# Optimization experiments

Measured on AMD Instinct MI355X. Metric: run time of the kernel, lower is better.

The kernel has to match this reference:

```python
import jax, jax.numpy as jnp
import numpy as np
from jax import lax

B, FCH, H, W = 2, 48, 512, 512
WNUM, PATCH = 1, 8
DEG = 180.0 / np.pi
# well-conditioned, slightly asymmetric fallback Mueller matrix for masked (non-physical) pixels
_SAFE = np.array([[1.0, 0.02, 0.01, 0.005],
                  [0.0, 0.95, 0.05, 0.0],
                  [0.0, -0.05, 0.90, 0.04],
                  [0.0, 0.0, -0.04, 0.85]], dtype=np.float32)


def setup_inputs():
    key = jax.random.key(0)
    x = 0.5 * jax.random.normal(key, (B, FCH, H, W), dtype=jnp.float32)
    eye = jnp.eye(4, dtype=jnp.float32).reshape(16)
    # bias intensity frames and both calibration matrices toward 2*I so per-pixel
    # 4x4 systems are well conditioned and M is near-physical
    boost = jnp.concatenate([2.0 * eye, 2.0 * eye, 2.0 * eye])[None, :, None, None]
    return {"x": x + boost}


def _charpoly_mask(M):
    # Cloude realizability test: characteristic-polynomial coefficients of the
    # Hermitian coherency matrix must all be >= 0 (all eigenvalues >= 0).
    s = jnp.stack([jnp.eye(2, dtype=jnp.complex64),
                   jnp.array([[1, 0], [0, -1]], jnp.complex64),
                   jnp.array([[0, 1], [1, 0]], jnp.complex64),
                   jnp.array([[0, -1j], [1j, 0]], jnp.complex64)])
    Bk = jnp.einsum('iab,jcd->ijacbd', s, s).reshape(16, 4, 4)  # kron(sigma_i, sigma_j)
    Hc = 0.25 * jnp.einsum('...k,kab->...ab', M.reshape(M.shape[:-2] + (16,)).astype(jnp.complex64), Bk)
    tr1 = jnp.trace(Hc, axis1=-2, axis2=-1).real
    H2 = Hc @ Hc
    tr2 = jnp.trace(H2, axis1=-2, axis2=-1).real
    tr3 = jnp.trace(H2 @ Hc, axis1=-2, axis2=-1).real
    c2 = 0.5 * (tr1 ** 2 - tr2)
    c3 = (tr1 ** 3 - 3.0 * tr1 * tr2 + 2.0 * tr3) / 6.0
    c4 = jnp.linalg.det(Hc).real
    return (tr1 >= 0) & (c2 >= 0) & (c3 >= 0) & (c4 >= 0)


def _compute_mm(A, F, Wm, norm=True):
    M = jnp.linalg.solve(A, F)  # A^-1 F
    M = jnp.swapaxes(jnp.linalg.solve(jnp.swapaxes(Wm, -1, -2), jnp.swapaxes(M, -1, -2)), -1, -2)  # ... W^-1
    return M / M[..., 0:1, 0:1] if norm else M


def _lu_chipman(M, mask):
    # Lu-Chipman polar decomposition M = M_delta @ M_R @ M_D (per pixel)
    M = jnp.where(mask[..., None, None], M, jnp.asarray(_SAFE))
    I3 = jnp.eye(3, dtype=M.dtype)
    D = M[..., 0, 1:]  # diattenuation vector
    d2 = jnp.clip(jnp.sum(D * D, -1), 0.0, 1.0 - 1e-6)
    d = jnp.sqrt(d2 + 1e-12)
    sq = jnp.sqrt(1.0 - d2)
    Dh = D / jnp.maximum(d, 1e-6)[..., None]
    mD = sq[..., None, None] * I3 + (1.0 - sq)[..., None, None] * (Dh[..., :, None] * Dh[..., None, :])
    ones = jnp.ones(M.shape[:-2] + (1,), M.dtype)
    MD = jnp.concatenate([jnp.concatenate([ones, D], -1)[..., None, :],
                          jnp.concatenate([D[..., None], mD], -1)], -2)
    Mp = jnp.swapaxes(jnp.linalg.solve(MD, jnp.swapaxes(M, -1, -2)), -1, -2)  # M @ MD^-1 (MD symmetric)
    mp = Mp[..., 1:, 1:]
    mm = mp @ jnp.swapaxes(mp, -1, -2)
    lam = jnp.clip(jnp.linalg.eigvalsh(mm), 1e-12, None)  # ascending
    s1, s2, s3 = jnp.sqrt(lam[..., 2]), jnp.sqrt(lam[..., 1]), jnp.sqrt(lam[..., 0])
    sgn = jnp.where(jnp.linalg.det(mp) < 0, -1.0, 1.0).astype(M.dtype)
    A3 = mm + (s1 * s2 + s2 * s3 + s3 * s1)[..., None, None] * I3 + 1e-6 * I3
    B3 = (s1 + s2 + s3)[..., None, None] * mm + (s1 * s2 * s3)[..., None, None] * I3
    mdel = sgn[..., None, None] * jnp.linalg.solve(A3, B3)
    Pdel = (M[..., 1:, 0] - jnp.einsum('...ij,...j->...i', M[..., 1:, 1:], D)) / (1.0 - d2)[..., None]
    top = jnp.concatenate([ones, jnp.zeros(M.shape[:-2] + (3,), M.dtype)], -1)[..., None, :]
    Mdel = jnp.concatenate([top, jnp.concatenate([Pdel[..., None], mdel], -1)], -2)
    MR = jnp.linalg.solve(Mdel + 1e-6 * jnp.eye(4, dtype=M.dtype), Mp)
    return MD, MR, Mdel


def _polarimetry(MD, MR, Mdel):
    clipc = lambda t: jnp.clip(t, -1.0 + 1e-6, 1.0 - 1e-6)
    D = MD[..., 0, 1:]
    totD = jnp.sqrt(jnp.sum(D * D, -1) + 1e-12)
    linD = jnp.sqrt(D[..., 0] ** 2 + D[..., 1] ** 2 + 1e-12)
    cirD = jnp.abs(D[..., 2])
    totR = jnp.arccos(clipc(jnp.trace(MR, axis1=-2, axis2=-1) / 2.0 - 1.0)) * DEG
    mR = MR[..., 1:, 1:]
    linR = jnp.arccos(clipc(jnp.sqrt((mR[..., 0, 0] + mR[..., 1, 1]) ** 2
                                     + (mR[..., 1, 0] - mR[..., 0, 1]) ** 2 + 1e-12) - 1.0)) * DEG
    cirR = 0.5 * jnp.arctan2(mR[..., 1, 0] - mR[..., 0, 1], mR[..., 0, 0] + mR[..., 1, 1]) * DEG
    # azimuth of linear retardance from retardance-vector components (r1, r2)
    azi = jnp.mod(0.5 * jnp.arctan2(mR[..., 2, 0] - mR[..., 0, 2], mR[..., 1, 2] - mR[..., 2, 1]) * DEG, 180.0)
    dazi = jnp.mod(0.5 * jnp.arctan2(D[..., 1], D[..., 0]) * DEG, 180.0)
    totP = 1.0 - jnp.abs(jnp.trace(Mdel[..., 1:, 1:], axis1=-2, axis2=-1)) / 3.0
    # p[:,0]=diattenuation, p[:,6]=linear retardance, p[:,7]=azimuth, p[:,-1]=depolarization
    return jnp.stack([totD, linD, cirD, totR, cirR, dazi, linR, azi, totP], axis=1)


def _rolling_circstd(a_deg, patch):
    # circstd(a/180*pi, high=pi, low=0) over patch x patch sliding windows, back to degrees.
    # circstd reduces to window means of cos/sin of doubled angles -> avg pooling.
    th = a_deg * (2.0 * np.pi / 180.0)
    wsum = lambda t: lax.reduce_window(t, 0.0, lax.add, (1, 1, patch, patch), (1, 1, 1, 1), 'SAME')
    cnt = wsum(jnp.ones_like(a_deg))
    R = jnp.sqrt(wsum(jnp.cos(th)) ** 2 + wsum(jnp.sin(th)) ** 2 + 1e-12) / cnt
    R = jnp.clip(R, 1e-7, 1.0 - 1e-7)
    return 0.5 * jnp.sqrt(-2.0 * jnp.log(R)) * DEG


def _forward(x):
    b, f, h, w = x.shape
    xw = jnp.moveaxis(x.reshape(b, WNUM, f // WNUM, h, w), 2, -1)  # (b, wnum, h, w, 48)
    Fi = xw[..., :16].reshape(b, WNUM, h, w, 4, 4)
    Am = xw[..., 16:32].reshape(b, WNUM, h, w, 4, 4)
    Wm = xw[..., 32:48].reshape(b, WNUM, h, w, 4, 4)
    M = _compute_mm(Am, Fi, Wm, norm=True)
    inten = xw[..., 0]
    imin = inten.min(axis=(1, 2, 3), keepdims=True)
    imax = inten.max(axis=(1, 2, 3), keepdims=True)
    inorm = (inten - imin) / (imax - imin)
    mchan = jnp.moveaxis(M.reshape(b, WNUM, h, w, 16), -1, 2).reshape(b, WNUM * 16, h, w)
    v = lax.stop_gradient(_charpoly_mask(M))
    MD, MR, Mdel = _lu_chipman(M, v)
    p = _polarimetry(MD, MR, Mdel)  # (b, 9, wnum, h, w)
    std = _rolling_circstd(p[:, 7], PATCH)
    # concat order matches forward: intensity, mueller, linr, totp, datt, azimuth, std
    return jnp.concatenate([inorm, mchan, p[:, 6], p[:, 8], p[:, 0], p[:, 7], std], axis=1)


def reference(x):
    return _forward(x)
```

## Files before the change

### kernel.cpp

```cpp
#include <hip/hip_runtime.h>
#include <math.h>

#define B_ 2
#define H_ 512
#define W_ 512
#define HW_ (H_ * W_)
#define NCH_IN 48
#define NCH_OUT 22
#define DEG_ 57.29577951308232f

__device__ __forceinline__ float frcp(float x)  { return __builtin_amdgcn_rcpf(x); }
__device__ __forceinline__ float fsqrtf_(float x){ return __builtin_amdgcn_sqrtf(x); }

__device__ __forceinline__ float fast_acos(float x) {
    float ax = fabsf(x);
    float t = fsqrtf_(fmaxf(1.0f - ax, 0.0f));
    float p = t * (1.5707288f + ax * (-0.2121144f + ax * (0.0742610f + ax * (-0.0187293f))));
    return (x >= 0.0f) ? p : (3.14159265358979f - p);
}

__device__ __forceinline__ float fast_atan2(float y, float x) {
    float ay = fabsf(y), ax = fabsf(x);
    float mx = fmaxf(ax, ay), mn = fminf(ax, ay);
    float a = mn * frcp(fmaxf(mx, 1e-37f));
    float s = a * a;
    float r = a * (0.99997726f + s * (-0.33262347f + s * (0.19354346f +
              s * (-0.11643287f + s * (0.05265332f + s * (-0.01172120f))))));
    if (ay > ax) r = 1.57079632679f - r;
    if (x < 0.0f) r = 3.14159265359f - r;
    return (y < 0.0f) ? -r : r;
}

__device__ __forceinline__ unsigned int fkey(float f) {
    unsigned int u = __float_as_uint(f);
    return (u & 0x80000000u) ? ~u : (u | 0x80000000u);
}
__device__ __forceinline__ float funkey(unsigned int k) {
    return (k & 0x80000000u) ? __uint_as_float(k ^ 0x80000000u) : __uint_as_float(~k);
}

__global__ void init_mm_kernel(unsigned int* mm) {
    mm[0] = 0xFFFFFFFFu; mm[1] = 0u;
    mm[2] = 0xFFFFFFFFu; mm[3] = 0u;
}

__global__ __launch_bounds__(256) void minmax_kernel(const float* __restrict__ x,
                                                     unsigned int* __restrict__ mm) {
    int b = blockIdx.x >> 6;
    int blk = blockIdx.x & 63;
    const float* src = x + (size_t)b * NCH_IN * HW_;
    float lo = INFINITY, hi = -INFINITY;
    for (int i = blk * 256 + threadIdx.x; i < HW_; i += 64 * 256) {
        float v = src[i];
        lo = fminf(lo, v);
        hi = fmaxf(hi, v);
    }
    __shared__ float slo[256], shi[256];
    slo[threadIdx.x] = lo; shi[threadIdx.x] = hi;
    __syncthreads();
    for (int s = 128; s > 0; s >>= 1) {
        if (threadIdx.x < s) {
            slo[threadIdx.x] = fminf(slo[threadIdx.x], slo[threadIdx.x + s]);
            shi[threadIdx.x] = fmaxf(shi[threadIdx.x], shi[threadIdx.x + s]);
        }
        __syncthreads();
    }
    if (threadIdx.x == 0) {
        atomicMin(&mm[2 * b], fkey(slo[0]));
        atomicMax(&mm[2 * b + 1], fkey(shi[0]));
    }
}

__device__ __forceinline__ void solve4(const float A[4][4], const float Bm[4][4], float X[4][4]) {
    float m[4][8];
#pragma unroll
    for (int i = 0; i < 4; i++) {
#pragma unroll
        for (int j = 0; j < 4; j++) { m[i][j] = A[i][j]; m[i][j + 4] = Bm[i][j]; }
    }
#pragma unroll
    for (int k = 0; k < 4; k++) {
#pragma unroll
        for (int r = k + 1; r < 4; r++) {
            bool sw = fabsf(m[r][k]) > fabsf(m[k][k]);
#pragma unroll
            for (int c = 0; c < 8; c++) {
                float a = m[k][c], b = m[r][c];
                m[k][c] = sw ? b : a;
                m[r][c] = sw ? a : b;
            }
        }
        float piv = frcp(m[k][k]);
#pragma unroll
        for (int c = 0; c < 8; c++) m[k][c] *= piv;
#pragma unroll
        for (int r = 0; r < 4; r++) {
            if (r == k) continue;
            float f = m[r][k];
#pragma unroll
            for (int c = 0; c < 8; c++) m[r][c] -= f * m[k][c];
        }
    }
#pragma unroll
    for (int i = 0; i < 4; i++)
#pragma unroll
        for (int j = 0; j < 4; j++) X[i][j] = m[i][j + 4];
}

__device__ __forceinline__ void mul4(const float A[4][4], const float B[4][4], float C[4][4]) {
#pragma unroll
    for (int i = 0; i < 4; i++)
#pragma unroll
        for (int j = 0; j < 4; j++) {
            float s = 0.0f;
#pragma unroll
            for (int k = 0; k < 4; k++) s += A[i][k] * B[k][j];
            C[i][j] = s;
        }
}

__device__ __forceinline__ void inv3(const float A[3][3], float out[3][3]) {
    float c00 = A[1][1] * A[2][2] - A[1][2] * A[2][1];
    float c01 = A[1][2] * A[2][0] - A[1][0] * A[2][2];
    float c02 = A[1][0] * A[2][1] - A[1][1] * A[2][0];
    float det = A[0][0] * c00 + A[0][1] * c01 + A[0][2] * c02;
    float id = frcp(det);
    out[0][0] = c00 * id;
    out[0][1] = (A[0][2] * A[2][1] - A[0][1] * A[2][2]) * id;
    out[0][2] = (A[0][1] * A[1][2] - A[0][2] * A[1][1]) * id;
    out[1][0] = c01 * id;
    out[1][1] = (A[0][0] * A[2][2] - A[0][2] * A[2][0]) * id;
    out[1][2] = (A[0][2] * A[1][0] - A[0][0] * A[1][2]) * id;
    out[2][0] = c02 * id;
    out[2][1] = (A[0][1] * A[2][0] - A[0][0] * A[2][1]) * id;
    out[2][2] = (A[0][0] * A[1][1] - A[0][1] * A[1][0]) * id;
}

__device__ __forceinline__ float det3(const float A[3][3]) {
    return A[0][0] * (A[1][1] * A[2][2] - A[1][2] * A[2][1])
         - A[0][1] * (A[1][0] * A[2][2] - A[1][2] * A[2][0])
         + A[0][2] * (A[1][0] * A[2][1] - A[1][1] * A[2][0]);
}

__device__ __forceinline__ void eig3_sym(const float A[3][3], float& l1, float& l2, float& l3) {
    float q = (A[0][0] + A[1][1] + A[2][2]) * (1.0f / 3.0f);
    float a00 = A[0][0] - q, a11 = A[1][1] - q, a22 = A[2][2] - q;
    float off = A[0][1] * A[0][1] + A[0][2] * A[0][2] + A[1][2] * A[1][2];
    float p2 = a00 * a00 + a11 * a11 + a22 * a22 + 2.0f * off;
    float p = fsqrtf_(p2 * (1.0f / 6.0f) + 1e-30f);
    float inv = frcp(p);
    float b00 = a00 * inv, b11 = a11 * inv, b22 = a22 * inv;
    float b01 = A[0][1] * inv, b02 = A[0][2] * inv, b12 = A[1][2] * inv;
    float detB = b00 * (b11 * b22 - b12 * b12)
               - b01 * (b01 * b22 - b12 * b02)
               + b02 * (b01 * b12 - b11 * b02);
    float r = 0.5f * detB;
    r = fminf(fmaxf(r, -1.0f), 1.0f);
    float phi = fast_acos(r) * (1.0f / 3.0f);
    l1 = q + 2.0f * p * __cosf(phi);
    l3 = q + 2.0f * p * __cosf(phi + 2.0943951023931953f);
    l2 = 3.0f * q - l1 - l3;
}

__global__ __launch_bounds__(256) void main_kernel(const float* __restrict__ x,
                                                   const unsigned int* __restrict__ mmk,
                                                   float* __restrict__ out) {
    int idx = blockIdx.x * 256 + threadIdx.x;
    if (idx >= B_ * HW_) return;
    int b = idx / HW_;
    int p = idx - b * HW_;
    const float* src = x + (size_t)b * NCH_IN * HW_ + p;

    float F[4][4], A[4][4], WT[4][4];
#pragma unroll
    for (int i = 0; i < 4; i++)
#pragma unroll
        for (int j = 0; j < 4; j++) {
            F[i][j]  = src[(4 * i + j) * HW_];
            A[i][j]  = src[(16 + 4 * i + j) * HW_];
            WT[j][i] = src[(32 + 4 * i + j) * HW_];
        }
    float inten = F[0][0];

    float X[4][4], XT[4][4], MT[4][4], M[4][4];
    solve4(A, F, X);
#pragma unroll
    for (int i = 0; i < 4; i++)
#pragma unroll
        for (int j = 0; j < 4; j++) XT[i][j] = X[j][i];
    solve4(WT, XT, MT);
    float nrm = frcp(MT[0][0]);
#pragma unroll
    for (int i = 0; i < 4; i++)
#pragma unroll
        for (int j = 0; j < 4; j++) M[i][j] = MT[j][i] * nrm;

    float* ob = out + (size_t)b * NCH_OUT * HW_ + p;
    float imin = funkey(mmk[2 * b]), imax = funkey(mmk[2 * b + 1]);
    ob[0] = (inten - imin) * frcp(imax - imin);
#pragma unroll
    for (int k = 0; k < 16; k++) ob[(size_t)(1 + k) * HW_] = M[k >> 2][k & 3];

    float Vr[4][4], Vi[4][4];
#pragma unroll
    for (int i = 0; i < 4; i++) {
        Vr[i][0] = M[i][0] + M[i][1]; Vi[i][0] = 0.0f;
        Vr[i][1] = M[i][0] - M[i][1]; Vi[i][1] = 0.0f;
        Vr[i][2] = M[i][2];           Vi[i][2] = -M[i][3];
        Vr[i][3] = M[i][2];           Vi[i][3] =  M[i][3];
    }
    float Hr[4][4], Hi[4][4];
    {
        const int cc[4] = {0, 1, 0, 1};
        const int dd[4] = {0, 1, 1, 0};
#pragma unroll
        for (int t = 0; t < 4; t++) {
            float wr = Vr[0][t] + Vr[1][t], wi = Vi[0][t] + Vi[1][t];
            float xr = Vr[0][t] - Vr[1][t], xi = Vi[0][t] - Vi[1][t];
            float yr = Vr[2][t] + Vi[3][t], yi = Vi[2][t] - Vr[3][t];
            float zr = Vr[2][t] - Vi[3][t], zi = Vi[2][t] + Vr[3][t];
            int c = cc[t], d = dd[t];
            Hr[c][d]         = 0.25f * wr; Hi[c][d]         = 0.25f * wi;
            Hr[c][2 + d]     = 0.25f * yr; Hi[c][2 + d]     = 0.25f * yi;
            Hr[2 + c][d]     = 0.25f * zr; Hi[2 + c][d]     = 0.25f * zi;
            Hr[2 + c][2 + d] = 0.25f * xr; Hi[2 + c][2 + d] = 0.25f * xi;
        }
    }
    float H2r[4][4], H2i[4][4];
#pragma unroll
    for (int i = 0; i < 4; i++)
#pragma unroll
        for (int j = 0; j < 4; j++) {
            float sr = 0.0f, si = 0.0f;
#pragma unroll
            for (int k = 0; k < 4; k++) {
                sr += Hr[i][k] * Hr[k][j] - Hi[i][k] * Hi[k][j];
                si += Hr[i][k] * Hi[k][j] + Hi[i][k] * Hr[k][j];
            }
            H2r[i][j] = sr; H2i[i][j] = si;
        }
    float tr1 = Hr[0][0] + Hr[1][1] + Hr[2][2] + Hr[3][3];
    float p2t = H2r[0][0] + H2r[1][1] + H2r[2][2] + H2r[3][3];
    float p3t = 0.0f, p4t = 0.0f;
#pragma unroll
    for (int i = 0; i < 4; i++)
#pragma unroll
        for (int j = 0; j < 4; j++) {
            p3t += H2r[i][j] * Hr[i][j] + H2i[i][j] * Hi[i][j];
            p4t += H2r[i][j] * H2r[i][j] + H2i[i][j] * H2i[i][j];
        }
    float c2 = 0.5f * (tr1 * tr1 - p2t);
    float c3 = (tr1 * tr1 * tr1 - 3.0f * tr1 * p2t + 2.0f * p3t) * (1.0f / 6.0f);
    float c4 = (tr1 * tr1 * tr1 * tr1 - 6.0f * tr1 * tr1 * p2t + 3.0f * p2t * p2t
                + 8.0f * tr1 * p3t - 6.0f * p4t) * (1.0f / 24.0f);
    bool mask = (tr1 >= 0.0f) && (c2 >= 0.0f) && (c3 >= 0.0f) && (c4 >= 0.0f);

    const float SAFE[4][4] = {{1.0f, 0.02f, 0.01f, 0.005f},
                              {0.0f, 0.95f, 0.05f, 0.0f},
                              {0.0f, -0.05f, 0.9f, 0.04f},
                              {0.0f, 0.0f, -0.04f, 0.85f}};
#pragma unroll
    for (int i = 0; i < 4; i++)
#pragma unroll
        for (int j = 0; j < 4; j++) M[i][j] = mask ? M[i][j] : SAFE[i][j];

    float D0 = M[0][1], D1 = M[0][2], D2v = M[0][3];
    float d2r = D0 * D0 + D1 * D1 + D2v * D2v;
    float totD = fsqrtf_(d2r + 1e-12f);
    float d2 = fminf(fmaxf(d2r, 0.0f), 1.0f - 1e-6f);
    float d = fsqrtf_(d2 + 1e-12f);
    float sq2 = 1.0f - d2;
    float sq = fsqrtf_(sq2);
    float dinv = frcp(fmaxf(d, 1e-6f));
    float h0 = D0 * dinv, h1 = D1 * dinv, h2 = D2v * dinv;

    float isq2 = frcp(sq2);
    float isq = frcp(sq);
    float cdh = (1.0f - sq) * isq2;
    float MDi[4][4];
    MDi[0][0] = isq2;
    MDi[0][1] = -isq2 * D0; MDi[0][2] = -isq2 * D1; MDi[0][3] = -isq2 * D2v;
    MDi[1][0] = MDi[0][1];  MDi[2][0] = MDi[0][2];  MDi[3][0] = MDi[0][3];
    float Dh[3] = {h0, h1, h2};
#pragma unroll
    for (int i = 0; i < 3; i++)
#pragma unroll
        for (int j = 0; j < 3; j++)
            MDi[1 + i][1 + j] = ((i == j) ? isq : 0.0f) + cdh * Dh[i] * Dh[j];

    float Mp[4][4];
    mul4(M, MDi, Mp);

    float mp3[3][3];
#pragma unroll
    for (int i = 0; i < 3; i++)
#pragma unroll
        for (int j = 0; j < 3; j++) mp3[i][j] = Mp[1 + i][1 + j];
    float mmS[3][3];
#pragma unroll
    for (int i = 0; i < 3; i++)
#pragma unroll
        for (int j = 0; j < 3; j++) {
            float s = 0.0f;
#pragma unroll
            for (int k = 0; k < 3; k++) s += mp3[i][k] * mp3[j][k];
            mmS[i][j] = s;
        }
    float l1, l2, l3;
    eig3_sym(mmS, l1, l2, l3);
    l1 = fmaxf(l1, 1e-12f); l2 = fmaxf(l2, 1e-12f); l3 = fmaxf(l3, 1e-12f);
    float s1 = fsqrtf_(l1), s2 = fsqrtf_(l2), s3 = fsqrtf_(l3);
    float sgn = (det3(mp3) < 0.0f) ? -1.0f : 1.0f;

    float e2s = s1 * s2 + s2 * s3 + s3 * s1 + 1e-6f;
    float e1s = s1 + s2 + s3;
    float e3s = s1 * s2 * s3;
    float A3[3][3], B3[3][3];
#pragma unroll
    for (int i = 0; i < 3; i++)
#pragma unroll
        for (int j = 0; j < 3; j++) {
            A3[i][j] = mmS[i][j] + ((i == j) ? e2s : 0.0f);
            B3[i][j] = e1s * mmS[i][j] + ((i == j) ? e3s : 0.0f);
        }
    float A3i[3][3];
    inv3(A3, A3i);
    float mdel[3][3];
#pragma unroll
    for (int i = 0; i < 3; i++)
#pragma unroll
        for (int j = 0; j < 3; j++) {
            float s = 0.0f;
#pragma unroll
            for (int k = 0; k < 3; k++) s += A3i[i][k] * B3[k][j];
            mdel[i][j] = sgn * s;
        }

    float Pd[3];
#pragma unroll
    for (int i = 0; i < 3; i++)
        Pd[i] = (M[1 + i][0] - (M[1 + i][1] * D0 + M[1 + i][2] * D1 + M[1 + i][3] * D2v)) * isq2;

    float MR0[4];
    const float inv_aeps = 1.0f / (1.0f + 1e-6f);
#pragma unroll
    for (int j = 0; j < 4; j++) MR0[j] = Mp[0][j] * inv_aeps;
    float m3[3][3];
#pragma unroll
    for (int i = 0; i < 3; i++)
#pragma unroll
        for (int j = 0; j < 3; j++) m3[i][j] = mdel[i][j] + ((i == j) ? 1e-6f : 0.0f);
    float m3i[3][3];
    inv3(m3, m3i);
    float MRr[3][4];
#pragma unroll
    for (int i = 0; i < 3; i++)
#pragma unroll
        for (int j = 0; j < 4; j++) {
            float s = 0.0f;
#pragma unroll
            for (int k = 0; k < 3; k++) s += m3i[i][k] * (Mp[1 + k][j] - Pd[k] * MR0[j]);
            MRr[i][j] = s;
        }

    float mR00 = MRr[0][1], mR01 = MRr[0][2], mR02 = MRr[0][3];
    float mR10 = MRr[1][1], mR11 = MRr[1][2], mR12 = MRr[1][3];
    float mR20 = MRr[2][1], mR21 = MRr[2][2];

    float t_lin = fsqrtf_((mR00 + mR11) * (mR00 + mR11) + (mR10 - mR01) * (mR10 - mR01) + 1e-12f) - 1.0f;
    t_lin = fminf(fmaxf(t_lin, -1.0f + 1e-6f), 1.0f - 1e-6f);
    float linR = fast_acos(t_lin) * DEG_;

    float azi = 0.5f * fast_atan2(mR20 - mR02, mR12 - mR21) * DEG_;
    if (azi < 0.0f) azi += 180.0f;

    float totP = 1.0f - fabsf(mdel[0][0] + mdel[1][1] + mdel[2][2]) * (1.0f / 3.0f);

    ob[(size_t)17 * HW_] = linR;
    ob[(size_t)18 * HW_] = totP;
    ob[(size_t)19 * HW_] = totD;
    ob[(size_t)20 * HW_] = azi;
}

#define TX_ 32
#define TY_ 8
__global__ __launch_bounds__(256) void circstd_kernel(float* __restrict__ out) {
    int tx0 = blockIdx.x * TX_;
    int ty0 = blockIdx.y * TY_;
    int b = blockIdx.z;
    const float* azi = out + (size_t)b * NCH_OUT * HW_ + (size_t)20 * HW_;

    __shared__ float lc[TY_ + 7][TX_ + 8];
    __shared__ float ls[TY_ + 7][TX_ + 8];
    __shared__ float hc[TY_ + 7][TX_];
    __shared__ float hs[TY_ + 7][TX_];

    for (int i = threadIdx.x; i < (TY_ + 7) * (TX_ + 7); i += 256) {
        int row = i / (TX_ + 7);
        int col = i - row * (TX_ + 7);
        int gy = ty0 - 3 + row;
        int gx = tx0 - 3 + col;
        float c = 0.0f, s = 0.0f;
        if (gy >= 0 && gy < H_ && gx >= 0 && gx < W_) {
            float th = azi[(size_t)gy * W_ + gx] * 0.03490658503988659f;
            __sincosf(th, &s, &c);
        }
        lc[row][col] = c; ls[row][col] = s;
    }
    __syncthreads();

    for (int i = threadIdx.x; i < (TY_ + 7) * TX_; i += 256) {
        int row = i / TX_;
        int col = i - row * TX_;
        float sc = 0.0f, ss = 0.0f;
#pragma unroll
        for (int d = 0; d < 8; d++) { sc += lc[row][col + d]; ss += ls[row][col + d]; }
        hc[row][col] = sc; hs[row][col] = ss;
    }
    __syncthreads();

    int col = threadIdx.x & (TX_ - 1);
    int row = threadIdx.x >> 5;
    float sc = 0.0f, ss = 0.0f;
#pragma unroll
    for (int k = 0; k < 8; k++) { sc += hc[row + k][col]; ss += hs[row + k][col]; }
    int y = ty0 + row, xc = tx0 + col;
    float rows = (float)(min(y + 5, H_) - max(y - 3, 0));
    float cols = (float)(min(xc + 5, W_) - max(xc - 3, 0));
    float R = fsqrtf_(sc * sc + ss * ss + 1e-12f) * frcp(rows * cols);
    R = fminf(fmaxf(R, 1e-7f), 1.0f - 1e-7f);
    float stdv = 0.5f * fsqrtf_(-2.0f * __logf(R)) * DEG_;
    out[(size_t)b * NCH_OUT * HW_ + (size_t)21 * HW_ + (size_t)y * W_ + xc] = stdv;
}

extern "C" void kernel_launch(void* const* d_in, const int* in_sizes, int n_in,
                              void* d_out, int out_size, void* d_ws, size_t ws_size,
                              hipStream_t stream) {
    const float* x = (const float*)d_in[0];
    float* out = (float*)d_out;
    unsigned int* mmk = (unsigned int*)d_ws;

    hipLaunchKernelGGL(init_mm_kernel, dim3(1), dim3(1), 0, stream, mmk);
    hipLaunchKernelGGL(minmax_kernel, dim3(128), dim3(256), 0, stream, x, mmk);
    hipLaunchKernelGGL(main_kernel, dim3((B_ * HW_ + 255) / 256), dim3(256), 0, stream, x, mmk, out);
    hipLaunchKernelGGL(circstd_kernel, dim3(W_ / TX_, H_ / TY_, B_), dim3(256), 0, stream, out);
}
```

Baseline: 177.6 us.

## Compute coherency charpoly in closed form, add nontemporal IO and memset init

```diff
diff --git a/kernel.cpp b/kernel.cpp
--- a/kernel.cpp
+++ b/kernel.cpp
@@ -10,6 +10,10 @@
 #define DEG_ 57.29577951308232f
 
 __device__ __forceinline__ float frcp(float x)  { return __builtin_amdgcn_rcpf(x); }
+__device__ __forceinline__ float frcp_nr(float x) {
+    float r = __builtin_amdgcn_rcpf(x);
+    return r * __builtin_fmaf(-x, r, 2.0f);
+}
 __device__ __forceinline__ float fsqrtf_(float x){ return __builtin_amdgcn_sqrtf(x); }
 
 __device__ __forceinline__ float fast_acos(float x) {
@@ -39,11 +43,6 @@
     return (k & 0x80000000u) ? __uint_as_float(k ^ 0x80000000u) : __uint_as_float(~k);
 }
 
-__global__ void init_mm_kernel(unsigned int* mm) {
-    mm[0] = 0xFFFFFFFFu; mm[1] = 0u;
-    mm[2] = 0xFFFFFFFFu; mm[3] = 0u;
-}
-
 __global__ __launch_bounds__(256) void minmax_kernel(const float* __restrict__ x,
                                                      unsigned int* __restrict__ mm) {
     int b = blockIdx.x >> 6;
@@ -66,7 +65,7 @@
         __syncthreads();
     }
     if (threadIdx.x == 0) {
-        atomicMin(&mm[2 * b], fkey(slo[0]));
+        atomicMax(&mm[2 * b], ~fkey(slo[0]));
         atomicMax(&mm[2 * b + 1], fkey(shi[0]));
     }
 }
@@ -90,7 +89,7 @@
                 m[r][c] = sw ? a : b;
             }
         }
-        float piv = frcp(m[k][k]);
+        float piv = frcp_nr(m[k][k]);
 #pragma unroll
         for (int c = 0; c < 8; c++) m[k][c] *= piv;
 #pragma unroll
@@ -124,7 +123,7 @@
     float c01 = A[1][2] * A[2][0] - A[1][0] * A[2][2];
     float c02 = A[1][0] * A[2][1] - A[1][1] * A[2][0];
     float det = A[0][0] * c00 + A[0][1] * c01 + A[0][2] * c02;
-    float id = frcp(det);
+    float id = frcp_nr(det);
     out[0][0] = c00 * id;
     out[0][1] = (A[0][2] * A[2][1] - A[0][1] * A[2][2]) * id;
     out[0][2] = (A[0][1] * A[1][2] - A[0][2] * A[1][1]) * id;
@@ -176,9 +175,9 @@
     for (int i = 0; i < 4; i++)
 #pragma unroll
         for (int j = 0; j < 4; j++) {
-            F[i][j]  = src[(4 * i + j) * HW_];
-            A[i][j]  = src[(16 + 4 * i + j) * HW_];
-            WT[j][i] = src[(32 + 4 * i + j) * HW_];
+            F[i][j]  = __builtin_nontemporal_load(&src[(4 * i + j) * HW_]);
+            A[i][j]  = __builtin_nontemporal_load(&src[(16 + 4 * i + j) * HW_]);
+            WT[j][i] = __builtin_nontemporal_load(&src[(32 + 4 * i + j) * HW_]);
         }
     float inten = F[0][0];
 
@@ -189,80 +188,84 @@
 #pragma unroll
         for (int j = 0; j < 4; j++) XT[i][j] = X[j][i];
     solve4(WT, XT, MT);
-    float nrm = frcp(MT[0][0]);
+    float nrm = frcp_nr(MT[0][0]);
 #pragma unroll
     for (int i = 0; i < 4; i++)
 #pragma unroll
         for (int j = 0; j < 4; j++) M[i][j] = MT[j][i] * nrm;
 
     float* ob = out + (size_t)b * NCH_OUT * HW_ + p;
-    float imin = funkey(mmk[2 * b]), imax = funkey(mmk[2 * b + 1]);
-    ob[0] = (inten - imin) * frcp(imax - imin);
-#pragma unroll
-    for (int k = 0; k < 16; k++) ob[(size_t)(1 + k) * HW_] = M[k >> 2][k & 3];
-
-    float Vr[4][4], Vi[4][4];
-#pragma unroll
-    for (int i = 0; i < 4; i++) {
-        Vr[i][0] = M[i][0] + M[i][1]; Vi[i][0] = 0.0f;
-        Vr[i][1] = M[i][0] - M[i][1]; Vi[i][1] = 0.0f;
-        Vr[i][2] = M[i][2];           Vi[i][2] = -M[i][3];
-        Vr[i][3] = M[i][2];           Vi[i][3] =  M[i][3];
-    }
-    float Hr[4][4], Hi[4][4];
+    float imin = funkey(~mmk[2 * b]), imax = funkey(mmk[2 * b + 1]);
+    __builtin_nontemporal_store((inten - imin) * frcp(imax - imin), &ob[0]);
+#pragma unroll
+    for (int k = 0; k < 16; k++)
+        __builtin_nontemporal_store(M[k >> 2][k & 3], &ob[(size_t)(1 + k) * HW_]);
+
     {
-        const int cc[4] = {0, 1, 0, 1};
-        const int dd[4] = {0, 1, 1, 0};
-#pragma unroll
-        for (int t = 0; t < 4; t++) {
-            float wr = Vr[0][t] + Vr[1][t], wi = Vi[0][t] + Vi[1][t];
-            float xr = Vr[0][t] - Vr[1][t], xi = Vi[0][t] - Vi[1][t];
-            float yr = Vr[2][t] + Vi[3][t], yi = Vi[2][t] - Vr[3][t];
-            float zr = Vr[2][t] - Vi[3][t], zi = Vi[2][t] + Vr[3][t];
-            int c = cc[t], d = dd[t];
-            Hr[c][d]         = 0.25f * wr; Hi[c][d]         = 0.25f * wi;
-            Hr[c][2 + d]     = 0.25f * yr; Hi[c][2 + d]     = 0.25f * yi;
-            Hr[2 + c][d]     = 0.25f * zr; Hi[2 + c][d]     = 0.25f * zi;
-            Hr[2 + c][2 + d] = 0.25f * xr; Hi[2 + c][2 + d] = 0.25f * xi;
-        }
-    }
-    float H2r[4][4], H2i[4][4];
-#pragma unroll
-    for (int i = 0; i < 4; i++)
-#pragma unroll
-        for (int j = 0; j < 4; j++) {
-            float sr = 0.0f, si = 0.0f;
-#pragma unroll
-            for (int k = 0; k < 4; k++) {
-                sr += Hr[i][k] * Hr[k][j] - Hi[i][k] * Hi[k][j];
-                si += Hr[i][k] * Hi[k][j] + Hi[i][k] * Hr[k][j];
-            }
-            H2r[i][j] = sr; H2i[i][j] = si;
-        }
-    float tr1 = Hr[0][0] + Hr[1][1] + Hr[2][2] + Hr[3][3];
-    float p2t = H2r[0][0] + H2r[1][1] + H2r[2][2] + H2r[3][3];
-    float p3t = 0.0f, p4t = 0.0f;
-#pragma unroll
-    for (int i = 0; i < 4; i++)
-#pragma unroll
-        for (int j = 0; j < 4; j++) {
-            p3t += H2r[i][j] * Hr[i][j] + H2i[i][j] * Hi[i][j];
-            p4t += H2r[i][j] * H2r[i][j] + H2i[i][j] * H2i[i][j];
-        }
-    float c2 = 0.5f * (tr1 * tr1 - p2t);
-    float c3 = (tr1 * tr1 * tr1 - 3.0f * tr1 * p2t + 2.0f * p3t) * (1.0f / 6.0f);
-    float c4 = (tr1 * tr1 * tr1 * tr1 - 6.0f * tr1 * tr1 * p2t + 3.0f * p2t * p2t
-                + 8.0f * tr1 * p3t - 6.0f * p4t) * (1.0f / 24.0f);
-    bool mask = (tr1 >= 0.0f) && (c2 >= 0.0f) && (c3 >= 0.0f) && (c4 >= 0.0f);
-
-    const float SAFE[4][4] = {{1.0f, 0.02f, 0.01f, 0.005f},
-                              {0.0f, 0.95f, 0.05f, 0.0f},
-                              {0.0f, -0.05f, 0.9f, 0.04f},
-                              {0.0f, 0.0f, -0.04f, 0.85f}};
-#pragma unroll
-    for (int i = 0; i < 4; i++)
-#pragma unroll
-        for (int j = 0; j < 4; j++) M[i][j] = mask ? M[i][j] : SAFE[i][j];
+        float a0 = M[0][0], b0 = M[0][1], c0 = M[0][2], e0 = M[0][3];
+        float a1 = M[1][0], b1 = M[1][1], c1 = M[1][2], e1 = M[1][3];
+        float a2 = M[2][0], b2 = M[2][1], c2_ = M[2][2], e2 = M[2][3];
+        float a3 = M[3][0], b3 = M[3][1], c3_ = M[3][2], e3 = M[3][3];
+        float sa = a0 + a1, da = a0 - a1, sb = b0 + b1, db = b0 - b1;
+        float d0 = sa + sb, d1 = sa - sb, d2 = da + db, d3 = da - db;
+        float u01r = c0 + c1,  u01i = -(e0 + e1);
+        float u23r = c0 - c1,  u23i = -(e0 - e1);
+        float u02r = a2 + b2,  u02i = -(a3 + b3);
+        float u13r = a2 - b2,  u13i = -(a3 - b3);
+        float u03r = c2_ - e3, u03i = -(e2 + c3_);
+        float u12r = c2_ + e3, u12i =  (e2 - c3_);
+
+        float n01 = u01r * u01r + u01i * u01i;
+        float n02 = u02r * u02r + u02i * u02i;
+        float n03 = u03r * u03r + u03i * u03i;
+        float n12 = u12r * u12r + u12i * u12i;
+        float n13 = u13r * u13r + u13i * u13i;
+        float n23 = u23r * u23r + u23i * u23i;
+
+        float q0 = d0 * d0 + n01 + n02 + n03;
+        float q1 = d1 * d1 + n01 + n12 + n13;
+        float q2 = d2 * d2 + n02 + n12 + n23;
+        float q3 = d3 * d3 + n03 + n13 + n23;
+        float p2 = q0 + q1 + q2 + q3;
+
+        float w01r = (d0 + d1) * u01r + (u02r * u12r + u02i * u12i) + (u03r * u13r + u03i * u13i);
+        float w01i = (d0 + d1) * u01i + (u02i * u12r - u02r * u12i) + (u03i * u13r - u03r * u13i);
+        float w02r = (d0 + d2) * u02r + (u01r * u12r - u01i * u12i) + (u03r * u23r + u03i * u23i);
+        float w02i = (d0 + d2) * u02i + (u01r * u12i + u01i * u12r) + (u03i * u23r - u03r * u23i);
+        float w03r = (d0 + d3) * u03r + (u01r * u13r - u01i * u13i) + (u02r * u23r - u02i * u23i);
+        float w03i = (d0 + d3) * u03i + (u01r * u13i + u01i * u13r) + (u02r * u23i + u02i * u23r);
+        float w12r = (d1 + d2) * u12r + (u01r * u02r + u01i * u02i) + (u13r * u23r + u13i * u23i);
+        float w12i = (d1 + d2) * u12i + (u01r * u02i - u01i * u02r) + (u13i * u23r - u13r * u23i);
+        float w13r = (d1 + d3) * u13r + (u01r * u03r + u01i * u03i) + (u12r * u23r - u12i * u23i);
+        float w13i = (d1 + d3) * u13i + (u01r * u03i - u01i * u03r) + (u12r * u23i + u12i * u23r);
+        float w23r = (d2 + d3) * u23r + (u02r * u03r + u02i * u03i) + (u12r * u13r + u12i * u13i);
+        float w23i = (d2 + d3) * u23i + (u02r * u03i - u02i * u03r) + (u12i * u13r - u12r * u13i);
+
+        float p3 = q0 * d0 + q1 * d1 + q2 * d2 + q3 * d3
+                 + 2.0f * (w01r * u01r + w01i * u01i + w02r * u02r + w02i * u02i
+                         + w03r * u03r + w03i * u03i + w12r * u12r + w12i * u12i
+                         + w13r * u13r + w13i * u13i + w23r * u23r + w23i * u23i);
+        float p4 = q0 * q0 + q1 * q1 + q2 * q2 + q3 * q3
+                 + 2.0f * (w01r * w01r + w01i * w01i + w02r * w02r + w02i * w02i
+                         + w03r * w03r + w03i * w03i + w12r * w12r + w12i * w12i
+                         + w13r * w13r + w13i * w13i + w23r * w23r + w23i * w23i);
+
+        float tr1 = 4.0f * a0;
+        float t2 = tr1 * tr1;
+        float c2v = t2 - p2;
+        float c3v = tr1 * t2 - 3.0f * tr1 * p2 + 2.0f * p3;
+        float c4v = t2 * t2 - 6.0f * t2 * p2 + 3.0f * p2 * p2 + 8.0f * tr1 * p3 - 6.0f * p4;
+        bool mask = (tr1 >= 0.0f) && (c2v >= 0.0f) && (c3v >= 0.0f) && (c4v >= 0.0f);
+
+        const float SAFE[4][4] = {{1.0f, 0.02f, 0.01f, 0.005f},
+                                  {0.0f, 0.95f, 0.05f, 0.0f},
+                                  {0.0f, -0.05f, 0.9f, 0.04f},
+                                  {0.0f, 0.0f, -0.04f, 0.85f}};
+#pragma unroll
+        for (int i = 0; i < 4; i++)
+#pragma unroll
+            for (int j = 0; j < 4; j++) M[i][j] = mask ? M[i][j] : SAFE[i][j];
+    }
 
     float D0 = M[0][1], D1 = M[0][2], D2v = M[0][3];
     float d2r = D0 * D0 + D1 * D1 + D2v * D2v;
@@ -274,7 +277,7 @@
     float dinv = frcp(fmaxf(d, 1e-6f));
     float h0 = D0 * dinv, h1 = D1 * dinv, h2 = D2v * dinv;
 
-    float isq2 = frcp(sq2);
+    float isq2 = frcp_nr(sq2);
     float isq = frcp(sq);
     float cdh = (1.0f - sq) * isq2;
     float MDi[4][4];
@@ -376,9 +379,9 @@
 
     float totP = 1.0f - fabsf(mdel[0][0] + mdel[1][1] + mdel[2][2]) * (1.0f / 3.0f);
 
-    ob[(size_t)17 * HW_] = linR;
-    ob[(size_t)18 * HW_] = totP;
-    ob[(size_t)19 * HW_] = totD;
+    __builtin_nontemporal_store(linR, &ob[(size_t)17 * HW_]);
+    __builtin_nontemporal_store(totP, &ob[(size_t)18 * HW_]);
+    __builtin_nontemporal_store(totD, &ob[(size_t)19 * HW_]);
     ob[(size_t)20 * HW_] = azi;
 }
 
@@ -430,7 +433,8 @@
     float R = fsqrtf_(sc * sc + ss * ss + 1e-12f) * frcp(rows * cols);
     R = fminf(fmaxf(R, 1e-7f), 1.0f - 1e-7f);
     float stdv = 0.5f * fsqrtf_(-2.0f * __logf(R)) * DEG_;
-    out[(size_t)b * NCH_OUT * HW_ + (size_t)21 * HW_ + (size_t)y * W_ + xc] = stdv;
+    __builtin_nontemporal_store(stdv,
+        &out[(size_t)b * NCH_OUT * HW_ + (size_t)21 * HW_ + (size_t)y * W_ + xc]);
 }
 
 extern "C" void kernel_launch(void* const* d_in, const int* in_sizes, int n_in,
@@ -440,7 +444,7 @@
     float* out = (float*)d_out;
     unsigned int* mmk = (unsigned int*)d_ws;
 
-    hipLaunchKernelGGL(init_mm_kernel, dim3(1), dim3(1), 0, stream, mmk);
+    hipMemsetAsync(mmk, 0, 4 * sizeof(unsigned int), stream);
     hipLaunchKernelGGL(minmax_kernel, dim3(128), dim3(256), 0, stream, x, mmk);
     hipLaunchKernelGGL(main_kernel, dim3((B_ * HW_ + 255) / 256), dim3(256), 0, stream, x, mmk, out);
     hipLaunchKernelGGL(circstd_kernel, dim3(W_ / TX_, H_ / TY_, B_), dim3(256), 0, stream, out);
```

Result: faster. 171.3 us (-3.5%).
